# Kernel tuning notes

Hardware: AMD Instinct MI355X
Metric: run time of the kernel (lower is better)

The kernel has to match this reference:

```python
import jax, jax.numpy as jnp
import numpy as np

H = 8        # heads
W = 64       # window size
SHIFT = True
DIM = 512
SCALE = (DIM // H) ** -0.5


def setup_inputs() -> dict:
    key = jax.random.key(0)
    k1, k2, k3, k4 = jax.random.split(key, 4)
    x = jax.random.normal(k1, (8, 4096, DIM), dtype=jnp.float32)
    w_qkv = jax.random.normal(k2, (3 * DIM, DIM), dtype=jnp.float32) * 0.02
    w_proj = jax.random.normal(k3, (DIM, DIM), dtype=jnp.float32) * 0.02
    b_proj = jax.random.normal(k4, (DIM,), dtype=jnp.float32) * 0.02
    return {"x": x, "w_qkv": w_qkv, "w_proj": w_proj, "b_proj": b_proj}


def reference(x, w_qkv, w_proj, b_proj):
    B, N, C = x.shape
    if SHIFT:
        x = jnp.roll(x, -W // 2, axis=1)
    pad = (W - N % W) % W  # static Python int
    if pad:
        x = jnp.pad(x, ((0, 0), (0, pad), (0, 0)))
    nw = x.shape[1] // W
    xw = x.reshape(B * nw, W, C)                     # (B', W, C)
    qkv = xw @ w_qkv.T                               # (B', W, 3C)
    qkv = qkv.reshape(B * nw, W, 3, H, C // H)
    q, k, v = qkv[:, :, 0], qkv[:, :, 1], qkv[:, :, 2]  # (B', W, H, dh)
    # NOTE: faithful to source -- heads are NOT moved before matmul, so
    # attention is over the head axis: attn shape (B', W, H, H).
    attn = jnp.einsum('bwhd,bwgd->bwhg', q, k) * SCALE
    attn = jax.nn.softmax(attn, axis=-1)
    out = jnp.einsum('bwhg,bwgd->bwhd', attn, v)     # (B', W, H, dh)
    # transpose(1,2) then raw reshape, exactly as torch does (channel scramble)
    out = out.transpose(0, 2, 1, 3).reshape(B * nw, W, C)
    out = out @ w_proj.T + b_proj
    out = out.reshape(B, nw * W, C)[:, :N]
    if SHIFT:
        out = jnp.roll(out, W // 2, axis=1)
    return out
```

## Files before the change

kernel.cpp:

```cpp
#include <hip/hip_runtime.h>
#include <math.h>

typedef __attribute__((ext_vector_type(8))) short short8;
typedef __attribute__((ext_vector_type(4))) float float4v;

#define KDIM  512
#define NQKV  1536

__device__ __forceinline__ unsigned short f2bf(float f) {
    unsigned int u = __float_as_uint(f);
    u += 0x7FFFu + ((u >> 16) & 1u);
    return (unsigned short)(u >> 16);
}
__device__ __forceinline__ float bf2f(unsigned short u) {
    return __uint_as_float(((unsigned int)u) << 16);
}

__device__ __forceinline__ void gl2lds16(const unsigned short* g, unsigned short* l) {
    __builtin_amdgcn_global_load_lds(
        (const __attribute__((address_space(1))) void*)g,
        (__attribute__((address_space(3))) void*)l, 16, 0, 0);
}

__global__ __launch_bounds__(256) void cast_x_kernel(const float* __restrict__ x,
                                                     unsigned short* __restrict__ xb) {
    int tid = blockIdx.x * 256 + threadIdx.x;
    int t = tid >> 7;
    int c = (tid & 127) << 2;
    int b = t >> 12, n = t & 4095;
    int src = (b << 12) | ((n + 32) & 4095);
    float4 v = *(const float4*)(x + (((size_t)src) << 9) + c);
    ushort4 o;
    o.x = f2bf(v.x); o.y = f2bf(v.y); o.z = f2bf(v.z); o.w = f2bf(v.w);
    *(ushort4*)(xb + (((size_t)t) << 9) + c) = o;
}

__global__ __launch_bounds__(256) void cast_w_kernel(const float* __restrict__ wqkv,
                                                     const float* __restrict__ wproj,
                                                     unsigned short* __restrict__ wqkvb,
                                                     unsigned short* __restrict__ wprojb) {
    int tid = blockIdx.x * 256 + threadIdx.x;
    int e = tid << 2;
    if (e < NQKV * KDIM) {
        float4 v = *(const float4*)(wqkv + e);
        ushort4 o; o.x = f2bf(v.x); o.y = f2bf(v.y); o.z = f2bf(v.z); o.w = f2bf(v.w);
        *(ushort4*)(wqkvb + e) = o;
    } else {
        int e2 = e - NQKV * KDIM;
        float4 v = *(const float4*)(wproj + e2);
        ushort4 o; o.x = f2bf(v.x); o.y = f2bf(v.y); o.z = f2bf(v.z); o.w = f2bf(v.w);
        *(ushort4*)(wprojb + e2) = o;
    }
}

template<int N, bool PROJ>
__global__ __launch_bounds__(256, 2) void gemm_kernel(
        const unsigned short* __restrict__ A,
        const unsigned short* __restrict__ B,
        unsigned short* __restrict__ Cb,
        float* __restrict__ Cf,
        const float* __restrict__ bias) {
    __shared__ __align__(16) unsigned short As[128 * 64];
    __shared__ __align__(16) unsigned short Bs[128 * 64];
    const int bn = blockIdx.x, bm = blockIdx.y;
    const int tid = threadIdx.x;
    const int wave = tid >> 6, lane = tid & 63;
    const int quad = lane >> 4, l16 = lane & 15;
    const int wm = (wave >> 1) * 64, wn = (wave & 1) * 64;
    const int srow = lane >> 3;
    const int scol = ((lane & 7) ^ srow) * 8;

    float4v acc[4][4] = {};

    const unsigned short* Abase = A + (size_t)(bm * 128) * KDIM;
    const unsigned short* Bbase = B + (size_t)(bn * 128) * KDIM;

    for (int k0 = 0; k0 < KDIM; k0 += 64) {
        #pragma unroll
        for (int j = 0; j < 4; j++) {
            int chunk = j * 4 + wave;
            int row = chunk * 8 + srow;
            gl2lds16(Abase + (size_t)row * KDIM + k0 + scol, As + chunk * 512);
            gl2lds16(Bbase + (size_t)row * KDIM + k0 + scol, Bs + chunk * 512);
        }
        __syncthreads();
        #pragma unroll
        for (int ki = 0; ki < 2; ki++) {
            short8 af[4], bf[4];
            #pragma unroll
            for (int mi = 0; mi < 4; mi++) {
                int r = wm + mi * 16 + l16;
                int blk = (ki * 4 + quad) ^ (l16 & 7);
                af[mi] = *(const short8*)(As + r * 64 + blk * 8);
            }
            #pragma unroll
            for (int ni = 0; ni < 4; ni++) {
                int r = wn + ni * 16 + l16;
                int blk = (ki * 4 + quad) ^ (l16 & 7);
                bf[ni] = *(const short8*)(Bs + r * 64 + blk * 8);
            }
            #pragma unroll
            for (int mi = 0; mi < 4; mi++)
                #pragma unroll
                for (int ni = 0; ni < 4; ni++)
                    acc[mi][ni] = __builtin_amdgcn_mfma_f32_16x16x32_bf16(
                        af[mi], bf[ni], acc[mi][ni], 0, 0, 0);
        }
        __syncthreads();
    }

    #pragma unroll
    for (int mi = 0; mi < 4; mi++) {
        #pragma unroll
        for (int r = 0; r < 4; r++) {
            int m = bm * 128 + wm + mi * 16 + quad * 4 + r;
            if (!PROJ) {
                #pragma unroll
                for (int ni = 0; ni < 4; ni++) {
                    int n = bn * 128 + wn + ni * 16 + l16;
                    Cb[(size_t)m * N + n] = f2bf(acc[mi][ni][r]);
                }
            } else {
                int b = m >> 12, p = m & 4095;
                int nrow = (p + 32) & 4095;
                float* orow = Cf + (((size_t)((b << 12) | nrow)) << 9);
                #pragma unroll
                for (int ni = 0; ni < 4; ni++) {
                    int n = bn * 128 + wn + ni * 16 + l16;
                    orow[n] = acc[mi][ni][r] + bias[n];
                }
            }
        }
    }
}

#define TPB_TOK 16
#define KV_STRIDE 1032
__global__ __launch_bounds__(128) void attn_kernel(const unsigned short* __restrict__ qkvb,
                                                   unsigned short* __restrict__ aob) {
    __shared__ __align__(16) unsigned short smem[TPB_TOK * KV_STRIDE];
    const int tid = threadIdx.x;
    const int t0 = blockIdx.x * TPB_TOK;
    const int tok = tid >> 3, h = tid & 7;
    const int t = t0 + tok;

    short8 qs[8];
    {
        const unsigned short* qsrc = qkvb + (size_t)t * NQKV + h * 64;
        #pragma unroll
        for (int dc = 0; dc < 8; dc++)
            qs[dc] = *(const short8*)(qsrc + dc * 8);
    }

    {
        int r = tid >> 3, cb = (tid & 7) * 8;
        const unsigned short* src = qkvb + (size_t)(t0 + r) * NQKV + 512;
        unsigned short* dst = smem + r * KV_STRIDE;
        #pragma unroll
        for (int p = 0; p < 16; p++) {
            int c = cb + p * 64;
            *(short8*)(dst + c) = *(const short8*)(src + c);
        }
    }
    __syncthreads();

    const unsigned short* row = smem + tok * KV_STRIDE;

    float qv[64];
    #pragma unroll
    for (int dc = 0; dc < 8; dc++)
        #pragma unroll
        for (int j = 0; j < 8; j++)
            qv[dc * 8 + j] = bf2f((unsigned short)qs[dc][j]);

    float s[8];
    #pragma unroll
    for (int g = 0; g < 8; g++) {
        float acc = 0.f;
        #pragma unroll
        for (int dc = 0; dc < 8; dc++) {
            short8 ks = *(const short8*)(row + g * 64 + dc * 8);
            #pragma unroll
            for (int j = 0; j < 8; j++)
                acc += qv[dc * 8 + j] * bf2f((unsigned short)ks[j]);
        }
        s[g] = acc;
    }

    float mx = s[0];
    #pragma unroll
    for (int g = 1; g < 8; g++) mx = fmaxf(mx, s[g]);
    float p[8], sum = 0.f;
    #pragma unroll
    for (int g = 0; g < 8; g++) { p[g] = __expf((s[g] - mx) * 0.125f); sum += p[g]; }
    float inv = 1.f / sum;
    #pragma unroll
    for (int g = 0; g < 8; g++) p[g] *= inv;

    float o[64];
    #pragma unroll
    for (int j = 0; j < 64; j++) o[j] = 0.f;
    #pragma unroll
    for (int g = 0; g < 8; g++) {
        #pragma unroll
        for (int dc = 0; dc < 8; dc++) {
            short8 vs = *(const short8*)(row + 512 + g * 64 + dc * 8);
            #pragma unroll
            for (int j = 0; j < 8; j++)
                o[dc * 8 + j] += p[g] * bf2f((unsigned short)vs[j]);
        }
    }

    int win = t >> 6, w = t & 63;
    unsigned short* dst = aob + (size_t)(win * 64 + h * 8 + (w >> 3)) * 512 + (w & 7) * 64;
    #pragma unroll
    for (int dc = 0; dc < 16; dc++) {
        ushort4 ov;
        ov.x = f2bf(o[dc * 4 + 0]); ov.y = f2bf(o[dc * 4 + 1]);
        ov.z = f2bf(o[dc * 4 + 2]); ov.w = f2bf(o[dc * 4 + 3]);
        *(ushort4*)(dst + dc * 4) = ov;
    }
}

extern "C" void kernel_launch(void* const* d_in, const int* in_sizes, int n_in,
                              void* d_out, int out_size, void* d_ws, size_t ws_size,
                              hipStream_t stream) {
    const float* x      = (const float*)d_in[0];
    const float* w_qkv  = (const float*)d_in[1];
    const float* w_proj = (const float*)d_in[2];
    const float* b_proj = (const float*)d_in[3];
    float* out = (float*)d_out;

    char* ws = (char*)d_ws;
    unsigned short* xb     = (unsigned short*)(ws);
    unsigned short* wqkvb  = (unsigned short*)(ws + 33554432);
    unsigned short* wprojb = (unsigned short*)(ws + 35127296);
    unsigned short* qkvb   = (unsigned short*)(ws + 35651584);
    unsigned short* aob    = (unsigned short*)(ws + 136314880);

    cast_x_kernel<<<16384, 256, 0, stream>>>(x, xb);
    cast_w_kernel<<<1024, 256, 0, stream>>>(w_qkv, w_proj, wqkvb, wprojb);
    gemm_kernel<NQKV, false><<<dim3(12, 256), 256, 0, stream>>>(xb, wqkvb, qkvb, nullptr, nullptr);
    attn_kernel<<<2048, 128, 0, stream>>>(qkvb, aob);
    gemm_kernel<512, true><<<dim3(4, 256), 256, 0, stream>>>(aob, wprojb, nullptr, out, b_proj);
}
```

Measured before the change: 250.1 us.

## Fuse x roll and bf16 cast into QKV GEMM and swizzle workgroups

Removes the separate cast_x kernel; the QKV GEMM now loads fp32 x rows with the window shift applied, converts to bf16 in registers and writes the A tile to LDS itself. Workgroup ids are remapped so each of eight consecutive-id groups covers a contiguous tile range, aiming at better L2 locality per die. This avoids a full write and re-read of a bf16 copy of x, at the cost of synchronous register-path loads with twice the bytes per A element instead of direct global-to-LDS loads.

```diff
diff --git a/kernel.cpp b/kernel.cpp
--- a/kernel.cpp
+++ b/kernel.cpp
@@ -20,19 +20,6 @@
     __builtin_amdgcn_global_load_lds(
         (const __attribute__((address_space(1))) void*)g,
         (__attribute__((address_space(3))) void*)l, 16, 0, 0);
-}
-
-__global__ __launch_bounds__(256) void cast_x_kernel(const float* __restrict__ x,
-                                                     unsigned short* __restrict__ xb) {
-    int tid = blockIdx.x * 256 + threadIdx.x;
-    int t = tid >> 7;
-    int c = (tid & 127) << 2;
-    int b = t >> 12, n = t & 4095;
-    int src = (b << 12) | ((n + 32) & 4095);
-    float4 v = *(const float4*)(x + (((size_t)src) << 9) + c);
-    ushort4 o;
-    o.x = f2bf(v.x); o.y = f2bf(v.y); o.z = f2bf(v.z); o.w = f2bf(v.w);
-    *(ushort4*)(xb + (((size_t)t) << 9) + c) = o;
 }
 
 __global__ __launch_bounds__(256) void cast_w_kernel(const float* __restrict__ wqkv,
@@ -56,13 +43,20 @@
 template<int N, bool PROJ>
 __global__ __launch_bounds__(256, 2) void gemm_kernel(
         const unsigned short* __restrict__ A,
+        const float* __restrict__ Ax,
         const unsigned short* __restrict__ B,
         unsigned short* __restrict__ Cb,
         float* __restrict__ Cf,
         const float* __restrict__ bias) {
     __shared__ __align__(16) unsigned short As[128 * 64];
     __shared__ __align__(16) unsigned short Bs[128 * 64];
-    const int bn = blockIdx.x, bm = blockIdx.y;
+    constexpr int GX  = N / 128;
+    constexpr int PER = (GX * 256) / 8;
+    const int wgid = blockIdx.y * GX + blockIdx.x;
+    const int swz  = (wgid & 7) * PER + (wgid >> 3);
+    const int bm = swz / GX;
+    const int bn = swz % GX;
+
     const int tid = threadIdx.x;
     const int wave = tid >> 6, lane = tid & 63;
     const int quad = lane >> 4, l16 = lane & 15;
@@ -72,15 +66,39 @@
 
     float4v acc[4][4] = {};
 
-    const unsigned short* Abase = A + (size_t)(bm * 128) * KDIM;
     const unsigned short* Bbase = B + (size_t)(bn * 128) * KDIM;
+    const unsigned short* Abase = PROJ ? (A + (size_t)(bm * 128) * KDIM) : nullptr;
+
+    const float* arow[4];
+    if (!PROJ) {
+        #pragma unroll
+        for (int j = 0; j < 4; j++) {
+            int chunk = j * 4 + wave;
+            int t = bm * 128 + chunk * 8 + srow;
+            int b = t >> 12, n = t & 4095;
+            int src = (b << 12) | ((n + 32) & 4095);
+            arow[j] = Ax + (((size_t)src) << 9) + scol;
+        }
+    }
 
     for (int k0 = 0; k0 < KDIM; k0 += 64) {
         #pragma unroll
         for (int j = 0; j < 4; j++) {
             int chunk = j * 4 + wave;
             int row = chunk * 8 + srow;
-            gl2lds16(Abase + (size_t)row * KDIM + k0 + scol, As + chunk * 512);
+            if (PROJ) {
+                gl2lds16(Abase + (size_t)row * KDIM + k0 + scol, As + chunk * 512);
+            } else {
+                const float* xs = arow[j] + k0;
+                float4 v0 = *(const float4*)xs;
+                float4 v1 = *(const float4*)(xs + 4);
+                short8 a8;
+                a8[0] = (short)f2bf(v0.x); a8[1] = (short)f2bf(v0.y);
+                a8[2] = (short)f2bf(v0.z); a8[3] = (short)f2bf(v0.w);
+                a8[4] = (short)f2bf(v1.x); a8[5] = (short)f2bf(v1.y);
+                a8[6] = (short)f2bf(v1.z); a8[7] = (short)f2bf(v1.w);
+                *(short8*)(As + chunk * 512 + lane * 8) = a8;
+            }
             gl2lds16(Bbase + (size_t)row * KDIM + k0 + scol, Bs + chunk * 512);
         }
         __syncthreads();
@@ -232,15 +250,13 @@
     float* out = (float*)d_out;
 
     char* ws = (char*)d_ws;
-    unsigned short* xb     = (unsigned short*)(ws);
     unsigned short* wqkvb  = (unsigned short*)(ws + 33554432);
     unsigned short* wprojb = (unsigned short*)(ws + 35127296);
     unsigned short* qkvb   = (unsigned short*)(ws + 35651584);
     unsigned short* aob    = (unsigned short*)(ws + 136314880);
 
-    cast_x_kernel<<<16384, 256, 0, stream>>>(x, xb);
     cast_w_kernel<<<1024, 256, 0, stream>>>(w_qkv, w_proj, wqkvb, wprojb);
-    gemm_kernel<NQKV, false><<<dim3(12, 256), 256, 0, stream>>>(xb, wqkvb, qkvb, nullptr, nullptr);
+    gemm_kernel<NQKV, false><<<dim3(12, 256), 256, 0, stream>>>(nullptr, x, wqkvb, qkvb, nullptr, nullptr);
     attn_kernel<<<2048, 128, 0, stream>>>(qkvb, aob);
-    gemm_kernel<512, true><<<dim3(4, 256), 256, 0, stream>>>(aob, wprojb, nullptr, out, b_proj);
-}
+    gemm_kernel<512, true><<<dim3(4, 256), 256, 0, stream>>>(aob, nullptr, wprojb, nullptr, out, b_proj);
+}
```

Measured after the change: 249.4 us. No clear change (-0.3%).
